# Kernel tuning notes

Measured on AMD Instinct MI355X. Metric: run time of the kernel, lower is better.

Reference implementation:

```python
import jax, jax.numpy as jnp
import numpy as np

TGT, BSZ, E, H, HD, P = 256, 64, 1024, 16, 64, 16
TAU = 3.0  # gumbel temperature
SCALE = 1.0 / np.sqrt(HD)


def setup_inputs() -> dict:
    rng = jax.random.key(0)
    ks = jax.random.split(rng, 14)
    n = lambda i, s: jax.random.normal(ks[i], s, dtype=jnp.float32)
    u = jax.random.uniform(ks[7], (BSZ, 2), dtype=jnp.float32, minval=1e-6, maxval=1.0 - 1e-6)
    return {
        'idx': 0,
        'query': n(0, (TGT, BSZ, E)),
        'key': n(1, (TGT, BSZ, E)),
        'value': n(2, (TGT, BSZ, E)),
        'prefix': n(3, (BSZ, 2, P, E)) * 0.5,  # gathered prefix_pool[prompt_ids]
        'batch_weight': jax.random.uniform(ks[4], (BSZ,), dtype=jnp.float32),
        'ori_image_features': n(5, (BSZ, 512)),
        'gumbel_noise': -jnp.log(-jnp.log(u)),  # standard gumbel(0,1) noise
        'in_proj_w': n(8, (3 * E, E)) * 0.02,
        'in_proj_b': jnp.zeros((3 * E,), jnp.float32),
        'out_w': n(9, (E, E)) * 0.02,
        'out_b': jnp.zeros((E,), jnp.float32),
        'gumbel_w': n(10, (2, 512)) * 0.05,
        'gumbel_b': jnp.zeros((2,), jnp.float32),
    }


def _sdpa(q, k, v):
    # q:[b,h,t,d] k,v:[b,h,s,d]
    s = jnp.einsum('bhtd,bhsd->bhts', q, k) * SCALE
    a = jax.nn.softmax(s, axis=-1)
    return jnp.einsum('bhts,bhsd->bhtd', a, v)


def reference(idx, query, key, value, prefix, batch_weight, ori_image_features,
              gumbel_noise, in_proj_w, in_proj_b, out_w, out_b, gumbel_w, gumbel_b):
    tgt, bsz, e = query.shape
    src = key.shape[0]
    # packed in-projection (w chunked into q/k/v blocks)
    w_q, w_k, w_v = jnp.split(in_proj_w, 3, axis=0)
    b_q, b_k, b_v = jnp.split(in_proj_b, 3, axis=0)
    q = query @ w_q.T + b_q            # [t,b,E]
    k = key @ w_k.T + b_k              # [s,b,E]
    v = value @ w_v.T + b_v
    # -> [b,h,t,d]
    q = q.reshape(tgt, bsz, H, HD).transpose(1, 2, 0, 3)
    k = k.reshape(src, bsz, H, HD).transpose(1, 2, 0, 3)
    v = v.reshape(src, bsz, H, HD).transpose(1, 2, 0, 3)
    # prefix k/v: [b,P,E] -> [b,h,P,d] (no in-projection, used raw as in source)
    pk = prefix[:, 0].reshape(bsz, P, H, HD).transpose(0, 2, 1, 3)
    pv = prefix[:, 1].reshape(bsz, P, H, HD).transpose(0, 2, 1, 3)

    attn = _sdpa(q, k, v)                      # [b,h,t,d]
    attn_flat = attn.transpose(2, 0, 1, 3).reshape(tgt * bsz, e)  # (t,b) row order

    attn_pre = _sdpa(q, pk, pv) * batch_weight[:, None, None, None]
    attn_pre_flat = attn_pre.transpose(2, 0, 1, 3).reshape(tgt * bsz, e)

    # gumbel-softmax gate (soft), one 2-way gate per sample
    logits = ori_image_features @ gumbel_w.T + gumbel_b           # [b,2]
    gumbel = jax.nn.softmax((logits + gumbel_noise) / TAU, axis=-1)
    gate = jnp.repeat(gumbel, tgt, axis=0)                        # [b*t,2] (b,t) order, as in source
    combined = attn_flat * gate[:, :1] + (attn_flat + attn_pre_flat) * gate[:, 1:2]

    out = combined @ out_w.T + out_b
    return out.reshape(tgt, bsz, e)
```

## Files before the change

kernel.cpp:

```cpp
#include <hip/hip_runtime.h>

typedef __attribute__((ext_vector_type(8))) short bf16x8;
typedef __attribute__((ext_vector_type(4))) float f32x4;
typedef __attribute__((ext_vector_type(8))) unsigned short ushort8;
typedef __attribute__((ext_vector_type(4))) unsigned short ushort4v;
typedef __attribute__((ext_vector_type(4))) float float4v;
typedef __attribute__((ext_vector_type(2))) unsigned int uint2v;

#define TGT 256
#define BSZ 64
#define EMB 1024
#define NH 16
#define HD 64
#define PP 16

__device__ __forceinline__ float b2f(unsigned short u) {
  return __builtin_bit_cast(float, ((unsigned int)u) << 16);
}
__device__ __forceinline__ unsigned short f2b(float f) {
  unsigned int u = __builtin_bit_cast(unsigned int, f);
  u += 0x7fffu + ((u >> 16) & 1u);
  return (unsigned short)(u >> 16);
}
__device__ __forceinline__ unsigned int pack2(float lo, float hi) {
  return (unsigned int)f2b(lo) | ((unsigned int)f2b(hi) << 16);
}
__device__ __forceinline__ f32x4 mfma16(bf16x8 a, bf16x8 b, f32x4 c) {
  return __builtin_amdgcn_mfma_f32_16x16x32_bf16(a, b, c, 0, 0, 0);
}
__device__ __forceinline__ void gl_lds16(const unsigned short* g, unsigned short* l) {
  __builtin_amdgcn_global_load_lds(
      (const __attribute__((address_space(1))) unsigned int*)g,
      (__attribute__((address_space(3))) unsigned int*)l, 16, 0, 0);
}

__global__ __launch_bounds__(64) void gate_kernel(
    const float* __restrict__ feat, const float* __restrict__ gw,
    const float* __restrict__ gb, const float* __restrict__ noise,
    float* __restrict__ g1) {
  const int b = blockIdx.x, lane = threadIdx.x;
  float a0 = 0.f, a1 = 0.f;
  for (int i = lane; i < 512; i += 64) {
    float f = feat[b * 512 + i];
    a0 += f * gw[i];
    a1 += f * gw[512 + i];
  }
#pragma unroll
  for (int off = 32; off >= 1; off >>= 1) {
    a0 += __shfl_xor(a0, off);
    a1 += __shfl_xor(a1, off);
  }
  if (lane == 0) {
    float l0 = (a0 + gb[0] + noise[b * 2 + 0]) * (1.0f / 3.0f);
    float l1 = (a1 + gb[1] + noise[b * 2 + 1]) * (1.0f / 3.0f);
    float mm = fmaxf(l0, l1);
    float e0 = __expf(l0 - mm), e1 = __expf(l1 - mm);
    g1[b] = e1 / (e0 + e1);
  }
}

__global__ __launch_bounds__(256) void cast_bf16_kernel(
    const float* __restrict__ in, unsigned short* __restrict__ out, int n8) {
  int i = blockIdx.x * blockDim.x + threadIdx.x;
  const int stride = gridDim.x * blockDim.x;
  for (; i < n8; i += stride) {
    const float4v* p = (const float4v*)(in + (size_t)i * 8);
    float4v v0 = p[0], v1 = p[1];
    ushort8 o = {f2b(v0[0]), f2b(v0[1]), f2b(v0[2]), f2b(v0[3]),
                 f2b(v1[0]), f2b(v1[1]), f2b(v1[2]), f2b(v1[3])};
    *(ushort8*)(out + (size_t)i * 8) = o;
  }
}

#define STAGE_A(s)                                       \
  {                                                      \
    int k0s = (s) * 32;                                  \
    unsigned short* d = &As[(s) & 3][wl];                \
    gl_lds16(a0p + k0s, d);                              \
    gl_lds16(a1p + k0s, d + 4096);                       \
  }
#define STAGE_B(s)                                       \
  {                                                      \
    int k0s = (s) * 32;                                  \
    unsigned short* d = &Bs[(s) & 3][wl];                \
    gl_lds16(b0p + k0s, d);                              \
    gl_lds16(b1p + k0s, d + 4096);                       \
  }
#define GEMM_STEP(s, DO_STAGE)                                        \
  {                                                                   \
    const unsigned short* Ab = &As[(s) & 3][0];                       \
    const unsigned short* Bb = &Bs[(s) & 3][0];                       \
    bf16x8 af[8], bfr[4];                                             \
    _Pragma("unroll") for (int mi = 0; mi < 8; ++mi)                  \
        af[mi] = *(const bf16x8*)&Ab[aoff + mi * 512];                \
    _Pragma("unroll") for (int ni = 0; ni < 2; ++ni)                  \
        bfr[ni] = *(const bf16x8*)&Bb[boff + ni * 512];               \
    if (DO_STAGE) STAGE_A((s) + 3);                                   \
    __builtin_amdgcn_s_barrier();                                     \
    __builtin_amdgcn_s_setprio(1);                                    \
    _Pragma("unroll") for (int mi = 0; mi < 8; ++mi) {                \
      acc[mi][0] = mfma16(af[mi], bfr[0], acc[mi][0]);                \
      acc[mi][1] = mfma16(af[mi], bfr[1], acc[mi][1]);                \
    }                                                                 \
    __builtin_amdgcn_s_setprio(0);                                    \
    __builtin_amdgcn_s_barrier();                                     \
    _Pragma("unroll") for (int ni = 2; ni < 4; ++ni)                  \
        bfr[ni] = *(const bf16x8*)&Bb[boff + ni * 512];               \
    if (DO_STAGE) STAGE_B((s) + 3);                                   \
    __builtin_amdgcn_s_barrier();                                     \
    __builtin_amdgcn_s_setprio(1);                                    \
    _Pragma("unroll") for (int mi = 0; mi < 8; ++mi) {                \
      acc[mi][2] = mfma16(af[mi], bfr[2], acc[mi][2]);                \
      acc[mi][3] = mfma16(af[mi], bfr[3], acc[mi][3]);                \
    }                                                                 \
    __builtin_amdgcn_s_setprio(0);                                    \
  }
#define STEP_WAIT(cntstr)                                \
  asm volatile("s_waitcnt " cntstr ::: "memory");        \
  __builtin_amdgcn_sched_barrier(0);                     \
  __builtin_amdgcn_s_barrier();

template <int OUT_F32, int QSCALE>
__global__ __launch_bounds__(512, 2) void gemm256_kernel(
    const unsigned short* __restrict__ A, const unsigned short* __restrict__ W,
    const float* __restrict__ bias, void* __restrict__ Cv) {
  constexpr int K = 1024, N = 1024;
  __shared__ __attribute__((aligned(16))) unsigned short As[4][8192];
  __shared__ __attribute__((aligned(16))) unsigned short Bs[4][8192];
  const int tid = threadIdx.x;
  const int wv = tid >> 6, lane = tid & 63;
  const int l15 = lane & 15, kg = lane >> 4;
  const int bid = blockIdx.x;
  const int cpx = gridDim.x >> 3;
  const int wg = (bid & 7) * cpx + (bid >> 3);
  const int m0 = (wg >> 2) * 256, n0 = (wg & 3) * 256;
  const int wmL = (wv >> 2) * 128, wnL = (wv & 3) * 64;

  const int sr = wv * 16 + (lane >> 2);
  const int sc = ((lane & 3) * 8) ^ (((sr >> 1) & 3) << 3);
  const unsigned short* a0p = A + (size_t)(m0 + sr) * K + sc;
  const unsigned short* a1p = a0p + (size_t)128 * K;
  const unsigned short* b0p = W + (size_t)(n0 + sr) * K + sc;
  const unsigned short* b1p = b0p + (size_t)128 * K;
  const int wl = wv * 512;

  const int x = ((l15 >> 1) & 3) << 3;
  const int aoff = (wmL + l15) * 32 + ((kg * 8) ^ x);
  const int boff = (wnL + l15) * 32 + ((kg * 8) ^ x);

  f32x4 acc[8][4];
#pragma unroll
  for (int i = 0; i < 8; ++i)
#pragma unroll
    for (int j = 0; j < 4; ++j) acc[i][j] = (f32x4){0.f, 0.f, 0.f, 0.f};

  STAGE_A(0); STAGE_B(0); STAGE_A(1); STAGE_B(1); STAGE_A(2); STAGE_B(2);
  STEP_WAIT("vmcnt(8)")

  for (int s = 0; s < 29; ++s) {
    GEMM_STEP(s, 1);
    STEP_WAIT("vmcnt(8)")
  }
  GEMM_STEP(29, 0);
  STEP_WAIT("vmcnt(4)")
  GEMM_STEP(30, 0);
  STEP_WAIT("vmcnt(0)")
  GEMM_STEP(31, 0);

#pragma unroll
  for (int mi = 0; mi < 8; ++mi) {
#pragma unroll
    for (int ni = 0; ni < 4; ++ni) {
      int col = n0 + wnL + ni * 16 + l15;
      float bcol = bias[col];
#pragma unroll
      for (int r = 0; r < 4; ++r) {
        int row = m0 + wmL + mi * 16 + kg * 4 + r;
        float v = acc[mi][ni][r] + bcol;
        if constexpr (QSCALE) v *= 0.125f;
        if constexpr (OUT_F32)
          ((float*)Cv)[(size_t)row * N + col] = v;
        else
          ((unsigned short*)Cv)[(size_t)row * N + col] = f2b(v);
      }
    }
  }
}

__global__ __launch_bounds__(512) void attn_kernel(
    const unsigned short* __restrict__ qb, const unsigned short* __restrict__ kb,
    const unsigned short* __restrict__ vb, const float* __restrict__ prefix,
    const float* __restrict__ bw, const float* __restrict__ g1,
    unsigned short* __restrict__ comb) {
  const int b = blockIdx.x, h = blockIdx.y;
  __shared__ __attribute__((aligned(16))) unsigned short Kl[256][64];
  __shared__ __attribute__((aligned(16))) unsigned short Vt[64 * 256];
  __shared__ __attribute__((aligned(16))) unsigned short PKl[16][64];
  __shared__ __attribute__((aligned(16))) unsigned short PVt[64][32];
  __shared__ __attribute__((aligned(16))) unsigned short Plds[8][16][40];
  unsigned short* Cb = &Kl[0][0];
  const int tid = threadIdx.x;

#pragma unroll
  for (int it = 0; it < 4; ++it) {
    int cid = tid + it * 512;
    int j = cid >> 3, c = cid & 7;
    size_t gro = (size_t)(j * BSZ + b) * EMB + h * HD + c * 8;
    *(ushort8*)&Kl[j][((c ^ (j & 7)) << 3)] = *(const ushort8*)(kb + gro);
    ushort8 vv = *(const ushort8*)(vb + gro);
#pragma unroll
    for (int i = 0; i < 8; ++i) {
      int gran = (j >> 3) ^ i ^ c;
      Vt[(c * 8 + i) * 256 + gran * 8 + (j & 7)] = vv[i];
    }
  }
  if (tid < 256) {
    int arr = tid >> 7, cid = tid & 127;
    int sp = cid >> 3, c = cid & 7;
    const float* src = prefix + ((size_t)(b * 2 + arr) * PP + sp) * EMB + h * HD + c * 8;
    float4v v0 = *(const float4v*)src;
    float4v v1 = *(const float4v*)(src + 4);
    if (arr == 0) {
      ushort8 o = {f2b(v0[0]), f2b(v0[1]), f2b(v0[2]), f2b(v0[3]),
                   f2b(v1[0]), f2b(v1[1]), f2b(v1[2]), f2b(v1[3])};
      *(ushort8*)&PKl[sp][((c ^ (sp & 7)) << 3)] = o;
    } else {
#pragma unroll
      for (int i = 0; i < 8; ++i)
        PVt[c * 8 + i][sp] = f2b(i < 4 ? v0[i] : v1[i - 4]);
    }
  } else if (tid < 384) {
    int cid = tid - 256;
    *(ushort8*)&PVt[cid >> 1][16 + (cid & 1) * 8] = (ushort8){0, 0, 0, 0, 0, 0, 0, 0};
  }
  __syncthreads();

  const int wv = tid >> 6, lane = tid & 63;
  const int l15 = lane & 15, g = lane >> 4;
  const int swl = l15 & 7;
  const float bwb = bw[b];
  unsigned short(&Pw)[16][40] = Plds[wv];

  const int t0 = wv * 32 + l15;
  const size_t qo0 = (size_t)(t0 * BSZ + b) * EMB + h * HD;
  const size_t qo1 = (size_t)((t0 + 16) * BSZ + b) * EMB + h * HD;
  bf16x8 qf[2][2];
  qf[0][0] = *(const bf16x8*)(qb + qo0 + g * 8);
  qf[0][1] = *(const bf16x8*)(qb + qo0 + 32 + g * 8);
  qf[1][0] = *(const bf16x8*)(qb + qo1 + g * 8);
  qf[1][1] = *(const bf16x8*)(qb + qo1 + 32 + g * 8);

  f32x4 O[2][4];
#pragma unroll
  for (int st = 0; st < 2; ++st)
#pragma unroll
    for (int dt = 0; dt < 4; ++dt) O[st][dt] = (f32x4){0.f, 0.f, 0.f, 0.f};
  float m[2] = {-3.0e38f, -3.0e38f}, l[2] = {0.f, 0.f};

#pragma unroll
  for (int ch = 0; ch < 8; ++ch) {
    const int rA = ch * 32 + l15, rB = rA + 16;
    bf16x8 ka0 = *(const bf16x8*)&Kl[rA][((g ^ swl) << 3)];
    bf16x8 ka1 = *(const bf16x8*)&Kl[rA][(((4 + g) ^ swl) << 3)];
    bf16x8 kb0 = *(const bf16x8*)&Kl[rB][((g ^ swl) << 3)];
    bf16x8 kb1 = *(const bf16x8*)&Kl[rB][(((4 + g) ^ swl) << 3)];
    f32x4 s[2][2];
#pragma unroll
    for (int st = 0; st < 2; ++st) {
      s[st][0] = (f32x4){0.f, 0.f, 0.f, 0.f};
      s[st][1] = (f32x4){0.f, 0.f, 0.f, 0.f};
      s[st][0] = mfma16(ka0, qf[st][0], s[st][0]);
      s[st][0] = mfma16(ka1, qf[st][1], s[st][0]);
      s[st][1] = mfma16(kb0, qf[st][0], s[st][1]);
      s[st][1] = mfma16(kb1, qf[st][1], s[st][1]);
    }
    bf16x8 pf[2];
#pragma unroll
    for (int st = 0; st < 2; ++st) {
      f32x4 sa = s[st][0], sb = s[st][1];
      float mx = fmaxf(fmaxf(fmaxf(sa[0], sa[1]), fmaxf(sa[2], sa[3])),
                       fmaxf(fmaxf(sb[0], sb[1]), fmaxf(sb[2], sb[3])));
      mx = fmaxf(mx, __shfl_xor(mx, 16));
      mx = fmaxf(mx, __shfl_xor(mx, 32));
      if (__ballot(mx > m[st] + 8.0f) != 0ull) {
        float mn = fmaxf(m[st], mx);
        float f = __expf(m[st] - mn);
        m[st] = mn;
        l[st] *= f;
#pragma unroll
        for (int dt = 0; dt < 4; ++dt)
#pragma unroll
          for (int r = 0; r < 4; ++r) O[st][dt][r] *= f;
      }
      float pA[4], pB[4];
#pragma unroll
      for (int r = 0; r < 4; ++r) {
        pA[r] = __expf(sa[r] - m[st]);
        pB[r] = __expf(sb[r] - m[st]);
      }
      uint2v wa = {pack2(pA[0], pA[1]), pack2(pA[2], pA[3])};
      uint2v wb2 = {pack2(pB[0], pB[1]), pack2(pB[2], pB[3])};
      *(uint2v*)&Pw[l15][g * 4] = wa;
      *(uint2v*)&Pw[l15][16 + g * 4] = wb2;
      float sloc = b2f((unsigned short)(wa[0] & 0xffff)) + b2f((unsigned short)(wa[0] >> 16)) +
                   b2f((unsigned short)(wa[1] & 0xffff)) + b2f((unsigned short)(wa[1] >> 16)) +
                   b2f((unsigned short)(wb2[0] & 0xffff)) + b2f((unsigned short)(wb2[0] >> 16)) +
                   b2f((unsigned short)(wb2[1] & 0xffff)) + b2f((unsigned short)(wb2[1] >> 16));
      l[st] += sloc;
      pf[st] = *(const bf16x8*)&Pw[l15][g * 8];
    }
#pragma unroll
    for (int dt = 0; dt < 4; ++dt) {
      const int drow = dt * 16 + l15;
      const int gran = (ch * 4 + g) ^ (drow & 7) ^ (drow >> 3);
      bf16x8 vf = *(const bf16x8*)&Vt[drow * 256 + gran * 8];
      O[0][dt] = mfma16(vf, pf[0], O[0][dt]);
      O[1][dt] = mfma16(vf, pf[1], O[1][dt]);
    }
  }

#pragma unroll
  for (int st = 0; st < 2; ++st) {
    float lf = l[st];
    lf += __shfl_xor(lf, 16);
    lf += __shfl_xor(lf, 32);
    float inv = 1.0f / lf;
#pragma unroll
    for (int dt = 0; dt < 4; ++dt)
#pragma unroll
      for (int r = 0; r < 4; ++r) O[st][dt][r] *= inv;
  }

  {
    bf16x8 pk0 = *(const bf16x8*)&PKl[l15][((g ^ swl) << 3)];
    bf16x8 pk1 = *(const bf16x8*)&PKl[l15][(((4 + g) ^ swl) << 3)];
    bf16x8 ppf[2];
#pragma unroll
    for (int st = 0; st < 2; ++st) {
      f32x4 sp4 = (f32x4){0.f, 0.f, 0.f, 0.f};
      sp4 = mfma16(pk0, qf[st][0], sp4);
      sp4 = mfma16(pk1, qf[st][1], sp4);
      float pm = fmaxf(fmaxf(sp4[0], sp4[1]), fmaxf(sp4[2], sp4[3]));
      pm = fmaxf(pm, __shfl_xor(pm, 16));
      pm = fmaxf(pm, __shfl_xor(pm, 32));
      float pe[4], pl = 0.f;
#pragma unroll
      for (int r = 0; r < 4; ++r) {
        pe[r] = __expf(sp4[r] - pm);
        pl += pe[r];
      }
      pl += __shfl_xor(pl, 16);
      pl += __shfl_xor(pl, 32);
      float cpre = g1[(t0 + 16 * st) >> 2] * bwb / pl;
#pragma unroll
      for (int r = 0; r < 4; ++r) pe[r] *= cpre;
      *(uint2v*)&Pw[l15][g * 4] = (uint2v){pack2(pe[0], pe[1]), pack2(pe[2], pe[3])};
      *(uint2v*)&Pw[l15][16 + g * 4] = (uint2v){0u, 0u};
      ppf[st] = *(const bf16x8*)&Pw[l15][g * 8];
    }
#pragma unroll
    for (int dt = 0; dt < 4; ++dt) {
      bf16x8 pvf = *(const bf16x8*)&PVt[dt * 16 + l15][g * 8];
      O[0][dt] = mfma16(pvf, ppf[0], O[0][dt]);
      O[1][dt] = mfma16(pvf, ppf[1], O[1][dt]);
    }
  }

  __syncthreads();
#pragma unroll
  for (int st = 0; st < 2; ++st) {
    int t = wv * 32 + st * 16 + l15;
#pragma unroll
    for (int dt = 0; dt < 4; ++dt) {
#pragma unroll
      for (int u = 0; u < 2; ++u) {
        unsigned int pw = pack2(O[st][dt][2 * u], O[st][dt][2 * u + 1]);
        int d = dt * 16 + g * 4 + 2 * u;
        *(unsigned int*)&Cb[t * 64 + (((d >> 3) ^ (t & 7)) << 3) + (d & 7)] = pw;
      }
    }
  }
  __syncthreads();
#pragma unroll
  for (int it = 0; it < 4; ++it) {
    int cid = tid + it * 512;
    int j = cid >> 3, c = cid & 7;
    ushort8 row = *(const ushort8*)&Cb[j * 64 + ((c ^ (j & 7)) << 3)];
    *(ushort8*)(comb + (size_t)(j * BSZ + b) * EMB + h * HD + c * 8) = row;
  }
}

extern "C" void kernel_launch(void* const* d_in, const int* in_sizes, int n_in,
                              void* d_out, int out_size, void* d_ws, size_t ws_size,
                              hipStream_t stream) {
  const float* query = (const float*)d_in[1];
  const float* key = (const float*)d_in[2];
  const float* value = (const float*)d_in[3];
  const float* prefix = (const float*)d_in[4];
  const float* bw = (const float*)d_in[5];
  const float* feat = (const float*)d_in[6];
  const float* noise = (const float*)d_in[7];
  const float* ipw = (const float*)d_in[8];
  const float* ipb = (const float*)d_in[9];
  const float* outw = (const float*)d_in[10];
  const float* outb = (const float*)d_in[11];
  const float* gw = (const float*)d_in[12];
  const float* gb = (const float*)d_in[13];
  float* out = (float*)d_out;

  char* ws = (char*)d_ws;
  const size_t MATB = (size_t)16384 * 1024;
  unsigned short* qb = (unsigned short*)ws;
  unsigned short* kb = qb + MATB;
  unsigned short* vb = kb + MATB;
  unsigned short* cb = vb + MATB;
  unsigned short* wip = cb + MATB;
  unsigned short* wo = wip + (size_t)3072 * 1024;
  float* g1 = (float*)(wo + (size_t)1024 * 1024);

  gate_kernel<<<64, 64, 0, stream>>>(feat, gw, gb, noise, g1);

  cast_bf16_kernel<<<1536, 256, 0, stream>>>(ipw, wip, 3072 * 1024 / 8);
  cast_bf16_kernel<<<512, 256, 0, stream>>>(outw, wo, 1024 * 1024 / 8);

  const int N8 = (int)(MATB / 8);
  cast_bf16_kernel<<<2048, 256, 0, stream>>>(query, cb, N8);
  gemm256_kernel<0, 1><<<256, 512, 0, stream>>>(cb, wip, ipb, qb);
  cast_bf16_kernel<<<2048, 256, 0, stream>>>(key, cb, N8);
  gemm256_kernel<0, 0><<<256, 512, 0, stream>>>(cb, wip + (size_t)1024 * 1024, ipb + 1024, kb);
  cast_bf16_kernel<<<2048, 256, 0, stream>>>(value, cb, N8);
  gemm256_kernel<0, 0><<<256, 512, 0, stream>>>(cb, wip + (size_t)2048 * 1024, ipb + 2048, vb);

  attn_kernel<<<dim3(64, 16), 512, 0, stream>>>(qb, kb, vb, prefix, bw, g1, cb);

  gemm256_kernel<1, 0><<<256, 512, 0, stream>>>(cb, wo, outb, out);
}
```

Baseline: 292.4 us.

## Store q/k/v and attention output in head-blocked layout for contiguous attention loads

The in-projection GEMM epilogue now writes bf16 outputs in a [batch][head][token][dim] layout. Each attention block can then load its K, V and Q slab contiguously, and K goes through direct global-to-LDS loads. The attention output is written in the same blocked layout, and the output-projection GEMM gains a blocked A-addressing mode to read it. This removes the strided 128-byte gathers in attention, at the cost of a more scattered per-element store pattern in the GEMM epilogue.

Result: faster. 279.0 us (-4.6%).

```diff
diff --git a/kernel.cpp b/kernel.cpp
--- a/kernel.cpp
+++ b/kernel.cpp
@@ -72,12 +72,13 @@
   }
 }
 
+#define AOFF(s) (A_BLOCKED ? (((s) >> 1) * 16384 + ((s)&1) * 32) : (s)*32)
 #define STAGE_A(s)                                       \
   {                                                      \
-    int k0s = (s) * 32;                                  \
+    const unsigned short* _ap = a0p + AOFF(s);           \
     unsigned short* d = &As[(s) & 3][wl];                \
-    gl_lds16(a0p + k0s, d);                              \
-    gl_lds16(a1p + k0s, d + 4096);                       \
+    gl_lds16(_ap, d);                                    \
+    gl_lds16(_ap + aD, d + 4096);                        \
   }
 #define STAGE_B(s)                                       \
   {                                                      \
@@ -120,7 +121,7 @@
   __builtin_amdgcn_sched_barrier(0);                     \
   __builtin_amdgcn_s_barrier();
 
-template <int OUT_F32, int QSCALE>
+template <int OUT_F32, int QSCALE, int A_BLOCKED>
 __global__ __launch_bounds__(512, 2) void gemm256_kernel(
     const unsigned short* __restrict__ A, const unsigned short* __restrict__ W,
     const float* __restrict__ bias, void* __restrict__ Cv) {
@@ -138,8 +139,13 @@
 
   const int sr = wv * 16 + (lane >> 2);
   const int sc = ((lane & 3) * 8) ^ (((sr >> 1) & 3) << 3);
-  const unsigned short* a0p = A + (size_t)(m0 + sr) * K + sc;
-  const unsigned short* a1p = a0p + (size_t)128 * K;
+  const int srg = m0 + sr;
+  const unsigned short* a0p;
+  if constexpr (A_BLOCKED)
+    a0p = A + (size_t)(srg & 63) * 262144 + (srg >> 6) * 64 + sc;
+  else
+    a0p = A + (size_t)srg * K + sc;
+  const int aD = A_BLOCKED ? 128 : 128 * K;
   const unsigned short* b0p = W + (size_t)(n0 + sr) * K + sc;
   const unsigned short* b1p = b0p + (size_t)128 * K;
   const int wl = wv * 512;
@@ -178,10 +184,12 @@
         int row = m0 + wmL + mi * 16 + kg * 4 + r;
         float v = acc[mi][ni][r] + bcol;
         if constexpr (QSCALE) v *= 0.125f;
-        if constexpr (OUT_F32)
+        if constexpr (OUT_F32) {
           ((float*)Cv)[(size_t)row * N + col] = v;
-        else
-          ((unsigned short*)Cv)[(size_t)row * N + col] = f2b(v);
+        } else {
+          int t = row >> 6, bb = row & 63, hh = col >> 6, dd = col & 63;
+          ((unsigned short*)Cv)[(size_t)((bb * 16 + hh) * 256 + t) * 64 + dd] = f2b(v);
+        }
       }
     }
   }
@@ -200,14 +208,16 @@
   __shared__ __attribute__((aligned(16))) unsigned short Plds[8][16][40];
   unsigned short* Cb = &Kl[0][0];
   const int tid = threadIdx.x;
+  const int wv = tid >> 6, lane = tid & 63;
+  const size_t slab = (size_t)(b * NH + h) * 16384;
 
 #pragma unroll
   for (int it = 0; it < 4; ++it) {
     int cid = tid + it * 512;
     int j = cid >> 3, c = cid & 7;
-    size_t gro = (size_t)(j * BSZ + b) * EMB + h * HD + c * 8;
-    *(ushort8*)&Kl[j][((c ^ (j & 7)) << 3)] = *(const ushort8*)(kb + gro);
-    ushort8 vv = *(const ushort8*)(vb + gro);
+    gl_lds16(kb + slab + (size_t)j * 64 + ((c ^ (j & 7)) << 3),
+             &Kl[0][0] + (size_t)(it * 512 + wv * 64) * 8);
+    ushort8 vv = *(const ushort8*)(vb + slab + (size_t)j * 64 + (c << 3));
 #pragma unroll
     for (int i = 0; i < 8; ++i) {
       int gran = (j >> 3) ^ i ^ c;
@@ -235,20 +245,18 @@
   }
   __syncthreads();
 
-  const int wv = tid >> 6, lane = tid & 63;
   const int l15 = lane & 15, g = lane >> 4;
   const int swl = l15 & 7;
   const float bwb = bw[b];
   unsigned short(&Pw)[16][40] = Plds[wv];
 
   const int t0 = wv * 32 + l15;
-  const size_t qo0 = (size_t)(t0 * BSZ + b) * EMB + h * HD;
-  const size_t qo1 = (size_t)((t0 + 16) * BSZ + b) * EMB + h * HD;
+  const size_t qbase = slab + (size_t)t0 * 64;
   bf16x8 qf[2][2];
-  qf[0][0] = *(const bf16x8*)(qb + qo0 + g * 8);
-  qf[0][1] = *(const bf16x8*)(qb + qo0 + 32 + g * 8);
-  qf[1][0] = *(const bf16x8*)(qb + qo1 + g * 8);
-  qf[1][1] = *(const bf16x8*)(qb + qo1 + 32 + g * 8);
+  qf[0][0] = *(const bf16x8*)(qb + qbase + g * 8);
+  qf[0][1] = *(const bf16x8*)(qb + qbase + 32 + g * 8);
+  qf[1][0] = *(const bf16x8*)(qb + qbase + 1024 + g * 8);
+  qf[1][1] = *(const bf16x8*)(qb + qbase + 1024 + 32 + g * 8);
 
   f32x4 O[2][4];
 #pragma unroll
@@ -386,7 +394,7 @@
     int cid = tid + it * 512;
     int j = cid >> 3, c = cid & 7;
     ushort8 row = *(const ushort8*)&Cb[j * 64 + ((c ^ (j & 7)) << 3)];
-    *(ushort8*)(comb + (size_t)(j * BSZ + b) * EMB + h * HD + c * 8) = row;
+    *(ushort8*)(comb + slab + (size_t)j * 64 + (c << 3)) = row;
   }
 }
 
@@ -425,13 +433,13 @@
 
   const int N8 = (int)(MATB / 8);
   cast_bf16_kernel<<<2048, 256, 0, stream>>>(query, cb, N8);
-  gemm256_kernel<0, 1><<<256, 512, 0, stream>>>(cb, wip, ipb, qb);
+  gemm256_kernel<0, 1, 0><<<256, 512, 0, stream>>>(cb, wip, ipb, qb);
   cast_bf16_kernel<<<2048, 256, 0, stream>>>(key, cb, N8);
-  gemm256_kernel<0, 0><<<256, 512, 0, stream>>>(cb, wip + (size_t)1024 * 1024, ipb + 1024, kb);
+  gemm256_kernel<0, 0, 0><<<256, 512, 0, stream>>>(cb, wip + (size_t)1024 * 1024, ipb + 1024, kb);
   cast_bf16_kernel<<<2048, 256, 0, stream>>>(value, cb, N8);
-  gemm256_kernel<0, 0><<<256, 512, 0, stream>>>(cb, wip + (size_t)2048 * 1024, ipb + 2048, vb);
+  gemm256_kernel<0, 0, 0><<<256, 512, 0, stream>>>(cb, wip + (size_t)2048 * 1024, ipb + 2048, vb);
 
   attn_kernel<<<dim3(64, 16), 512, 0, stream>>>(qb, kb, vb, prefix, bw, g1, cb);
 
-  gemm256_kernel<1, 0><<<256, 512, 0, stream>>>(cb, wo, outb, out);
-}
+  gemm256_kernel<1, 0, 1><<<256, 512, 0, stream>>>(cb, wo, outb, out);
+}
```
